# Performance work log

Hardware: AMD Instinct MI355X
Metric: run time of the kernel (lower is better)

## Reference

```python
import jax, jax.numpy as jnp
import numpy as np

B, L, G, K, HID, CLS = 256, 1000, 300, 19, 100, 2  # batch, seq len, num_cnns, kernel, per-unit hidden, classes
P = L // 10  # pooled length = per-group input features = 100
EPS = 1e-5


def setup_inputs() -> dict:
    key = jax.random.key(0)
    ks = jax.random.split(key, 24)
    u = lambda k, s: jax.random.uniform(k, s, jnp.float32, 0.5, 1.5)
    n = lambda k, s, sc=0.1: jax.random.normal(k, s, jnp.float32) * sc
    return {
        "x": jax.random.normal(ks[0], (B, 4, L), jnp.float32),
        # motif scanner conv: [out=G, in=4, k=19]
        "conv_w": n(ks[1], (G, 4, K)),
        "conv_b": n(ks[2], (G,)),
        "bn1_g": u(ks[3], (G,)), "bn1_b": n(ks[4], (G,)),
        "bn1_m": n(ks[5], (G,)), "bn1_v": u(ks[6], (G,)),
        # grouped 1x1 conv #1: per-group [HID <- P]
        "W1": n(ks[7], (G, HID, P)),
        "b1": n(ks[8], (G, HID)),
        "bn2_g": u(ks[9], (G, HID)), "bn2_b": n(ks[10], (G, HID)),
        "bn2_m": n(ks[11], (G, HID)), "bn2_v": u(ks[12], (G, HID)),
        # grouped 1x1 conv #2: per-group [1 <- HID]
        "W2": n(ks[13], (G, HID)),
        "b2": n(ks[14], (G,)),
        "bn3_g": u(ks[15], (G,)), "bn3_b": n(ks[16], (G,)),
        "bn3_m": n(ks[17], (G,)), "bn3_v": u(ks[18], (G,)),
        # final classifier Linear(G, CLS)
        "cls_w": n(ks[19], (CLS, G)),
        "cls_b": n(ks[20], (CLS,)),
    }


def reference(x, conv_w, conv_b, bn1_g, bn1_b, bn1_m, bn1_v,
              W1, b1, bn2_g, bn2_b, bn2_m, bn2_v,
              W2, b2, bn3_g, bn3_b, bn3_m, bn3_v,
              cls_w, cls_b):
    # Conv1d(4->G, k=19, pad=9): same-length output [B, G, L]
    h = jax.lax.conv_general_dilated(
        x, conv_w, window_strides=(1,), padding=[(K // 2, K // 2)],
        dimension_numbers=("NCH", "OIH", "NCH")) + conv_b[None, :, None]
    # BatchNorm1d (inference) + ReLU
    s1 = bn1_g / jnp.sqrt(bn1_v + EPS)
    h = jax.nn.relu((h - bn1_m[None, :, None]) * s1[None, :, None] + bn1_b[None, :, None])
    # MaxPool1d(10): L divisible by 10 -> reshape-max  [B, G, P]
    h = h.reshape(B, G, P, 10).max(-1)
    # Flatten+Unsqueeze+grouped 1x1 conv == block-diagonal matmul per group
    h1 = jnp.einsum("bgi,ghi->bgh", h, W1) + b1            # [B, G, HID]
    h1 = jax.nn.relu((h1 - bn2_m) * (bn2_g / jnp.sqrt(bn2_v + EPS)) + bn2_b)
    # Dropout(0.3) is identity at inference
    h2 = jnp.einsum("bgh,gh->bg", h1, W2) + b2             # [B, G]
    h2 = jax.nn.relu((h2 - bn3_m) * (bn3_g / jnp.sqrt(bn3_v + EPS)) + bn3_b)
    # classifier
    return h2 @ cls_w.T + cls_b                            # [B, CLS]
```

## Files before the change

kernel.cpp:

```cpp
#include <hip/hip_runtime.h>


typedef unsigned short ushort_t;
typedef short short8 __attribute__((ext_vector_type(8)));
typedef float floatx4 __attribute__((ext_vector_type(4)));

constexpr float EPSf = 1e-5f;

__device__ __forceinline__ ushort_t f2bf(float f) {
    unsigned u = __float_as_uint(f);
    unsigned r = (u + 0x7FFFu + ((u >> 16) & 1u)) >> 16;
    return (ushort_t)r;
}

constexpr int T1_BLKS = 8320;
constexpr int T2_BLKS = 114;
constexpr int T3_BLKS = 4200;
__global__ __launch_bounds__(256) void prep_all(
    const float* __restrict__ x, const float* __restrict__ conv_w, const float* __restrict__ W1,
    ushort_t* __restrict__ xph, ushort_t* __restrict__ Wc, ushort_t* __restrict__ W1b)
{
    const int blk = blockIdx.x, t = threadIdx.x;
    if (blk < T1_BLKS) {
        int u = blk * 256 + t;
        int iu = u % 520, r = u / 520;
        int c = r & 3, phi = (r >> 2) & 3, b = r >> 4;
        int src = iu * 2 + phi - 9;
        const float* xb = x + b * 4000 + c * 1000;
        float v0 = ((unsigned)src < 1000u) ? xb[src] : 0.f;
        float v1 = ((unsigned)(src + 1) < 1000u) ? xb[src + 1] : 0.f;
        ((unsigned*)xph)[u] = (unsigned)f2bf(v0) | ((unsigned)f2bf(v1) << 16);
    } else if (blk < T1_BLKS + T2_BLKS) {
        int idx = (blk - T1_BLKS) * 256 + t;
        int j = idx & 7, g = (idx >> 3) % 304, kc = idx / (304 * 8);
        int k = kc * 8 + j, c = k / 24, tt = k - c * 24;
        float v = (g < 300 && tt < 19) ? conv_w[g * 76 + c * 19 + tt] : 0.f;
        Wc[idx] = f2bf(v);
    } else {
        int v = (blk - T1_BLKS - T2_BLKS) * 256 + t;
        int jj = v & 1, r = v >> 1;
        int h = r % 112, r2 = r / 112;
        int kc = r2 & 15, g = r2 >> 4;
        int i0 = kc * 8 + jj * 4;
        ushort4 o = make_ushort4(0, 0, 0, 0);
        if (h < 100 && i0 <= 96) {
            float4 w = *(const float4*)&W1[(size_t)g * 10000 + h * 100 + i0];
            o = make_ushort4(f2bf(w.x), f2bf(w.y), f2bf(w.z), f2bf(w.w));
        }
        *(ushort4*)&W1b[((size_t)(g * 16 + kc) * 112 + h) * 8 + jj * 4] = o;
    }
}

__global__ __launch_bounds__(448, 2) void conv_mfma(
    const ushort_t* __restrict__ xph, const ushort_t* __restrict__ Wc,
    const float* __restrict__ conv_b, const float* __restrict__ g1, const float* __restrict__ be1,
    const float* __restrict__ m1, const float* __restrict__ v1,
    ushort_t* __restrict__ pooled)
{
    __shared__ ushort_t Wl[12 * 304 * 8];
    __shared__ ushort_t xl[16 * 1040];
    __shared__ float A1s[304], B1s[304];

    const int tid = threadIdx.x;
    const int b = blockIdx.x;

    {
        const uint4* wsrc = (const uint4*)Wc;
        uint4* wdst = (uint4*)Wl;
        for (int i = tid; i < 3648; i += 448) wdst[i] = wsrc[i];
        const uint4* xsrc = (const uint4*)(xph + (size_t)b * 16640);
        uint4* xdst = (uint4*)xl;
        for (int i = tid; i < 2080; i += 448) xdst[i] = xsrc[i];
        if (tid < 304) {
            if (tid < 300) {
                float A = g1[tid] * rsqrtf(v1[tid] + EPSf);
                A1s[tid] = A;
                B1s[tid] = (conv_b[tid] - m1[tid]) * A + be1[tid];
            } else { A1s[tid] = 0.f; B1s[tid] = 0.f; }
        }
    }
    __syncthreads();

    const int w = tid >> 6, lane = tid & 63;
    const int p0 = w * 16;
    const int row = lane & 15, quad = lane >> 4;
    const int p_r = p0 + row;
    const int prc = (p_r < 100) ? p_r : 99;

    uint4 af[10][3];
#pragma unroll
    for (int s = 0; s < 3; ++s) {
        int k0 = s * 32 + quad * 8;
        int c = k0 / 24, t0 = k0 - c * 24;
        int base0 = 10 * prc + t0;
        const ushort_t* xc = &xl[c * 1040];
#pragma unroll
        for (int d = 0; d < 10; ++d) {
            int base = base0 + d;
            int phi = base & 3, bi = base - phi;
            const ushort_t* p = xc + phi * 4160 + bi;
            uint2 lo = *(const uint2*)p;
            uint2 hi = *(const uint2*)(p + 4);
            af[d][s] = (uint4){lo.x, lo.y, hi.x, hi.y};
        }
    }

    for (int gt = 0; gt < 19; ++gt) {
        short8 bf[3];
#pragma unroll
        for (int s = 0; s < 3; ++s) {
            uint4 t4 = *(const uint4*)&Wl[(((s * 4 + quad) * 304) + gt * 16 + row) * 8];
            bf[s] = __builtin_bit_cast(short8, t4);
        }
        const float a1v = A1s[gt * 16 + row], b1v = B1s[gt * 16 + row];
        floatx4 mx = {0.f, 0.f, 0.f, 0.f};
#pragma unroll
        for (int d = 0; d < 10; ++d) {
            floatx4 acc = {0.f, 0.f, 0.f, 0.f};
#pragma unroll
            for (int s = 0; s < 3; ++s)
                acc = __builtin_amdgcn_mfma_f32_16x16x32_bf16(
                    __builtin_bit_cast(short8, af[d][s]), bf[s], acc, 0, 0, 0);
#pragma unroll
            for (int r = 0; r < 4; ++r)
                mx[r] = fmaxf(mx[r], fmaf(acc[r], a1v, b1v));
        }
        const int g = gt * 16 + row;
        const int pr0 = p0 + quad * 4;
        if (g < 300 && pr0 < 100) {
            ushort4 o = make_ushort4(f2bf(mx[0]), f2bf(mx[1]), f2bf(mx[2]), f2bf(mx[3]));
            *(ushort4*)&pooled[((size_t)b * 300 + g) * 100 + pr0] = o;
        }
    }
}

__global__ __launch_bounds__(256, 2) void mlp_mfma(
    const ushort_t* __restrict__ pooled, const ushort_t* __restrict__ W1b,
    const float* __restrict__ b1, const float* __restrict__ g2, const float* __restrict__ be2,
    const float* __restrict__ m2, const float* __restrict__ v2,
    const float* __restrict__ W2, const float* __restrict__ b2,
    const float* __restrict__ g3, const float* __restrict__ be3,
    const float* __restrict__ m3, const float* __restrict__ v3,
    float* __restrict__ h2ws)
{
    __shared__ ushort_t W1l[16 * 112 * 8];
    __shared__ ushort_t pl[128 * 128];
    __shared__ float A2s[112], C2s[112], w2sl[112];
    __shared__ float sA3, sC3;

    const int tid = threadIdx.x;
    const int g = blockIdx.y, b0 = blockIdx.x * 128;

    {
        const uint4* src = (const uint4*)(W1b + (size_t)g * 14336);
        uint4* dst = (uint4*)W1l;
        for (int i = tid; i < 1792; i += 256) dst[i] = src[i];
    }
    for (int q = tid; q < 128 * 16; q += 256) {
        int bl = q >> 4, kc = q & 15;
        const ushort_t* src = pooled + ((size_t)(b0 + bl) * 300 + g) * 100 + kc * 8;
        uint2 lo = *(const uint2*)src;
        uint2 hi = *(const uint2*)(src + 4);
        int swz = kc ^ (bl & 7);
        *(uint4*)&pl[((bl * 16) + swz) * 8] = (uint4){lo.x, lo.y, hi.x, hi.y};
    }
    if (tid < 112) {
        float a2 = 0.f, c2 = 0.f, w2v = 0.f;
        if (tid < 100) {
            int q = g * 100 + tid;
            a2 = g2[q] * rsqrtf(v2[q] + EPSf);
            c2 = (b1[q] - m2[q]) * a2 + be2[q];
            w2v = W2[q];
        }
        A2s[tid] = a2; C2s[tid] = c2; w2sl[tid] = w2v;
    }
    if (tid == 0) {
        float a3 = g3[g] * rsqrtf(v3[g] + EPSf);
        sA3 = a3; sC3 = (b2[g] - m3[g]) * a3 + be3[g];
    }
    __syncthreads();

    const int w = tid >> 6, lane = tid & 63;
    const int col = lane & 15, quad = lane >> 4;

    short8 bfr[7][4];
#pragma unroll
    for (int nt = 0; nt < 7; ++nt)
#pragma unroll
        for (int s = 0; s < 4; ++s) {
            uint4 t4 = *(const uint4*)&W1l[(((s * 4 + quad) * 112) + nt * 16 + col) * 8];
            bfr[nt][s] = __builtin_bit_cast(short8, t4);
        }

#pragma unroll
    for (int mi = 0; mi < 2; ++mi) {
        const int mt = w * 2 + mi;
        const int bl = mt * 16 + col;
        uint4 afr[4];
#pragma unroll
        for (int s = 0; s < 4; ++s) {
            int kc = s * 4 + quad;
            afr[s] = *(const uint4*)&pl[((bl * 16) + (kc ^ (bl & 7))) * 8];
        }
        float run0 = 0.f, run1 = 0.f, run2 = 0.f, run3 = 0.f;
#pragma unroll
        for (int nt = 0; nt < 7; ++nt) {
            floatx4 acc = {0.f, 0.f, 0.f, 0.f};
#pragma unroll
            for (int s = 0; s < 4; ++s)
                acc = __builtin_amdgcn_mfma_f32_16x16x32_bf16(
                    __builtin_bit_cast(short8, afr[s]), bfr[nt][s], acc, 0, 0, 0);
            const float a2v = A2s[nt * 16 + col], c2v = C2s[nt * 16 + col], w2v = w2sl[nt * 16 + col];
            run0 += fmaxf(fmaf(acc[0], a2v, c2v), 0.f) * w2v;
            run1 += fmaxf(fmaf(acc[1], a2v, c2v), 0.f) * w2v;
            run2 += fmaxf(fmaf(acc[2], a2v, c2v), 0.f) * w2v;
            run3 += fmaxf(fmaf(acc[3], a2v, c2v), 0.f) * w2v;
        }
#pragma unroll
        for (int m = 1; m <= 8; m <<= 1) {
            run0 += __shfl_xor(run0, m, 64);
            run1 += __shfl_xor(run1, m, 64);
            run2 += __shfl_xor(run2, m, 64);
            run3 += __shfl_xor(run3, m, 64);
        }
        if (col == 0) {
            float4 o;
            o.x = fmaxf(fmaf(run0, sA3, sC3), 0.f);
            o.y = fmaxf(fmaf(run1, sA3, sC3), 0.f);
            o.z = fmaxf(fmaf(run2, sA3, sC3), 0.f);
            o.w = fmaxf(fmaf(run3, sA3, sC3), 0.f);
            *(float4*)&h2ws[g * 256 + b0 + mt * 16 + quad * 4] = o;
        }
    }
}

__global__ __launch_bounds__(64) void classifier_kernel(
    const float* __restrict__ h2ws, const float* __restrict__ cls_w,
    const float* __restrict__ cls_b, float* __restrict__ out) {
    const int b = blockIdx.x, t = threadIdx.x;
    float a0 = 0.f, a1 = 0.f;
    for (int gg = t; gg < 300; gg += 64) {
        float v = h2ws[gg * 256 + b];
        a0 = fmaf(v, cls_w[gg], a0);
        a1 = fmaf(v, cls_w[300 + gg], a1);
    }
#pragma unroll
    for (int off = 32; off; off >>= 1) {
        a0 += __shfl_down(a0, off);
        a1 += __shfl_down(a1, off);
    }
    if (t == 0) {
        out[b * 2 + 0] = a0 + cls_b[0];
        out[b * 2 + 1] = a1 + cls_b[1];
    }
}

extern "C" void kernel_launch(void* const* d_in, const int* in_sizes, int n_in,
                              void* d_out, int out_size, void* d_ws, size_t ws_size,
                              hipStream_t stream) {
    const float* x      = (const float*)d_in[0];
    const float* conv_w = (const float*)d_in[1];
    const float* conv_b = (const float*)d_in[2];
    const float* bn1_g  = (const float*)d_in[3];
    const float* bn1_b  = (const float*)d_in[4];
    const float* bn1_m  = (const float*)d_in[5];
    const float* bn1_v  = (const float*)d_in[6];
    const float* W1     = (const float*)d_in[7];
    const float* b1     = (const float*)d_in[8];
    const float* bn2_g  = (const float*)d_in[9];
    const float* bn2_b  = (const float*)d_in[10];
    const float* bn2_m  = (const float*)d_in[11];
    const float* bn2_v  = (const float*)d_in[12];
    const float* W2     = (const float*)d_in[13];
    const float* b2     = (const float*)d_in[14];
    const float* bn3_g  = (const float*)d_in[15];
    const float* bn3_b  = (const float*)d_in[16];
    const float* bn3_m  = (const float*)d_in[17];
    const float* bn3_v  = (const float*)d_in[18];
    const float* cls_w  = (const float*)d_in[19];
    const float* cls_b  = (const float*)d_in[20];

    char* wsb = (char*)d_ws;
    ushort_t* pooled = (ushort_t*)(wsb);
    ushort_t* xph    = (ushort_t*)(wsb + 15360000);
    ushort_t* Wc     = (ushort_t*)(wsb + 23879680);
    ushort_t* W1b    = (ushort_t*)(wsb + 23938048);
    float*    h2ws   = (float*)  (wsb + 32539648);

    prep_all<<<dim3(T1_BLKS + T2_BLKS + T3_BLKS), 256, 0, stream>>>(x, conv_w, W1, xph, Wc, W1b);

    conv_mfma<<<dim3(256), 448, 0, stream>>>(
        xph, Wc, conv_b, bn1_g, bn1_b, bn1_m, bn1_v, pooled);

    mlp_mfma<<<dim3(2, 300), 256, 0, stream>>>(
        pooled, W1b, b1, bn2_g, bn2_b, bn2_m, bn2_v, W2, b2,
        bn3_g, bn3_b, bn3_m, bn3_v, h2ws);

    classifier_kernel<<<dim3(256), 64, 0, stream>>>(h2ws, cls_w, cls_b, (float*)d_out);
}
```

Before: 152.2 us.

## Fuse input phase-split into conv kernel, split conv over two halves, XCD-aware block mapping

The bf16 phase-split of x now happens inside the conv kernel, so the global xph intermediate and its large prep pass are gone. Each batch's conv work is split across two blocks along the pooled axis (52 and 48 positions), using 256 threads and a smaller LDS tile, which gives twice as many blocks. The W1 prep and MLP kernels remap block indices so that all blocks for one group land on the same XCD, aiming for L2 reuse of W1b and pooled data. The cost is some redundant x loads at the halo overlap and some idle blocks and wavefronts in the XCD mapping and the second conv half.

```diff
diff --git a/kernel.cpp b/kernel.cpp
--- a/kernel.cpp
+++ b/kernel.cpp
@@ -13,34 +13,28 @@
     return (ushort_t)r;
 }
 
-constexpr int T1_BLKS = 8320;
-constexpr int T2_BLKS = 114;
-constexpr int T3_BLKS = 4200;
+constexpr int WC_BLKS  = 114;
+constexpr int W1B_BLKS = 4256;
 __global__ __launch_bounds__(256) void prep_all(
-    const float* __restrict__ x, const float* __restrict__ conv_w, const float* __restrict__ W1,
-    ushort_t* __restrict__ xph, ushort_t* __restrict__ Wc, ushort_t* __restrict__ W1b)
+    const float* __restrict__ conv_w, const float* __restrict__ W1,
+    ushort_t* __restrict__ Wc, ushort_t* __restrict__ W1b)
 {
     const int blk = blockIdx.x, t = threadIdx.x;
-    if (blk < T1_BLKS) {
-        int u = blk * 256 + t;
-        int iu = u % 520, r = u / 520;
-        int c = r & 3, phi = (r >> 2) & 3, b = r >> 4;
-        int src = iu * 2 + phi - 9;
-        const float* xb = x + b * 4000 + c * 1000;
-        float v0 = ((unsigned)src < 1000u) ? xb[src] : 0.f;
-        float v1 = ((unsigned)(src + 1) < 1000u) ? xb[src + 1] : 0.f;
-        ((unsigned*)xph)[u] = (unsigned)f2bf(v0) | ((unsigned)f2bf(v1) << 16);
-    } else if (blk < T1_BLKS + T2_BLKS) {
-        int idx = (blk - T1_BLKS) * 256 + t;
+    if (blk < WC_BLKS) {
+        int idx = blk * 256 + t;
         int j = idx & 7, g = (idx >> 3) % 304, kc = idx / (304 * 8);
         int k = kc * 8 + j, c = k / 24, tt = k - c * 24;
         float v = (g < 300 && tt < 19) ? conv_w[g * 76 + c * 19 + tt] : 0.f;
         Wc[idx] = f2bf(v);
     } else {
-        int v = (blk - T1_BLKS - T2_BLKS) * 256 + t;
+        int blk2 = blk - WC_BLKS;
+        int xcd = blk2 & 7, j = blk2 >> 3;
+        int gl = j / 14, inner = j - gl * 14;
+        int g = xcd * 38 + gl;
+        if (g >= 300) return;
+        int v = inner * 256 + t;
         int jj = v & 1, r = v >> 1;
-        int h = r % 112, r2 = r / 112;
-        int kc = r2 & 15, g = r2 >> 4;
+        int h = r % 112, kc = r / 112;
         int i0 = kc * 8 + jj * 4;
         ushort4 o = make_ushort4(0, 0, 0, 0);
         if (h < 100 && i0 <= 96) {
@@ -51,54 +45,62 @@
     }
 }
 
-__global__ __launch_bounds__(448, 2) void conv_mfma(
-    const ushort_t* __restrict__ xph, const ushort_t* __restrict__ Wc,
+__global__ __launch_bounds__(256, 2) void conv_mfma(
+    const float* __restrict__ x, const ushort_t* __restrict__ Wc,
     const float* __restrict__ conv_b, const float* __restrict__ g1, const float* __restrict__ be1,
     const float* __restrict__ m1, const float* __restrict__ v1,
     ushort_t* __restrict__ pooled)
 {
     __shared__ ushort_t Wl[12 * 304 * 8];
-    __shared__ ushort_t xl[16 * 1040];
+    __shared__ ushort_t xl[16 * 552];
     __shared__ float A1s[304], B1s[304];
 
     const int tid = threadIdx.x;
-    const int b = blockIdx.x;
-
+    const int b = blockIdx.x, q = blockIdx.y;
+    const int X0 = q * 520;
+
+    for (int u = tid; u < 16 * 276; u += 256) {
+        int iu = u % 276, r = u / 276;
+        int c = r & 3, phi = r >> 2;
+        int gi = X0 + 2 * iu + phi - 9;
+        const float* xb = x + b * 4000 + c * 1000;
+        float v0 = ((unsigned)gi < 1000u) ? xb[gi] : 0.f;
+        float v1_ = ((unsigned)(gi + 1) < 1000u) ? xb[gi + 1] : 0.f;
+        ((unsigned*)xl)[u] = (unsigned)f2bf(v0) | ((unsigned)f2bf(v1_) << 16);
+    }
     {
         const uint4* wsrc = (const uint4*)Wc;
         uint4* wdst = (uint4*)Wl;
-        for (int i = tid; i < 3648; i += 448) wdst[i] = wsrc[i];
-        const uint4* xsrc = (const uint4*)(xph + (size_t)b * 16640);
-        uint4* xdst = (uint4*)xl;
-        for (int i = tid; i < 2080; i += 448) xdst[i] = xsrc[i];
-        if (tid < 304) {
-            if (tid < 300) {
-                float A = g1[tid] * rsqrtf(v1[tid] + EPSf);
-                A1s[tid] = A;
-                B1s[tid] = (conv_b[tid] - m1[tid]) * A + be1[tid];
-            } else { A1s[tid] = 0.f; B1s[tid] = 0.f; }
-        }
+        for (int i = tid; i < 3648; i += 256) wdst[i] = wsrc[i];
+    }
+    for (int i = tid; i < 304; i += 256) {
+        if (i < 300) {
+            float A = g1[i] * rsqrtf(v1[i] + EPSf);
+            A1s[i] = A;
+            B1s[i] = (conv_b[i] - m1[i]) * A + be1[i];
+        } else { A1s[i] = 0.f; B1s[i] = 0.f; }
     }
     __syncthreads();
 
     const int w = tid >> 6, lane = tid & 63;
-    const int p0 = w * 16;
+    if (q == 1 && w == 3) return;
+    const int p0 = q ? (52 + w * 16) : (w * 16);
+    const int pmax = q ? 99 : 51;
     const int row = lane & 15, quad = lane >> 4;
     const int p_r = p0 + row;
-    const int prc = (p_r < 100) ? p_r : 99;
+    const int prc = (p_r < pmax) ? p_r : pmax;
 
     uint4 af[10][3];
 #pragma unroll
     for (int s = 0; s < 3; ++s) {
         int k0 = s * 32 + quad * 8;
         int c = k0 / 24, t0 = k0 - c * 24;
-        int base0 = 10 * prc + t0;
-        const ushort_t* xc = &xl[c * 1040];
+        int base0 = 10 * prc + t0 - X0;
 #pragma unroll
         for (int d = 0; d < 10; ++d) {
-            int base = base0 + d;
-            int phi = base & 3, bi = base - phi;
-            const ushort_t* p = xc + phi * 4160 + bi;
+            int local = base0 + d;
+            int phi = local & 3, bi = local - phi;
+            const ushort_t* p = &xl[(phi * 4 + c) * 552 + bi];
             uint2 lo = *(const uint2*)p;
             uint2 hi = *(const uint2*)(p + 4);
             af[d][s] = (uint4){lo.x, lo.y, hi.x, hi.y};
@@ -127,7 +129,7 @@
         }
         const int g = gt * 16 + row;
         const int pr0 = p0 + quad * 4;
-        if (g < 300 && pr0 < 100) {
+        if (g < 300 && pr0 + 3 <= pmax) {
             ushort4 o = make_ushort4(f2bf(mx[0]), f2bf(mx[1]), f2bf(mx[2]), f2bf(mx[3]));
             *(ushort4*)&pooled[((size_t)b * 300 + g) * 100 + pr0] = o;
         }
@@ -149,7 +151,11 @@
     __shared__ float sA3, sC3;
 
     const int tid = threadIdx.x;
-    const int g = blockIdx.y, b0 = blockIdx.x * 128;
+    const int blk = blockIdx.x;
+    const int xcd = blk & 7, j = blk >> 3;
+    const int g = xcd * 38 + (j >> 1);
+    if (g >= 300) return;
+    const int b0 = (j & 1) * 128;
 
     {
         const uint4* src = (const uint4*)(W1b + (size_t)g * 14336);
@@ -167,10 +173,10 @@
     if (tid < 112) {
         float a2 = 0.f, c2 = 0.f, w2v = 0.f;
         if (tid < 100) {
-            int q = g * 100 + tid;
-            a2 = g2[q] * rsqrtf(v2[q] + EPSf);
-            c2 = (b1[q] - m2[q]) * a2 + be2[q];
-            w2v = W2[q];
+            int qq = g * 100 + tid;
+            a2 = g2[qq] * rsqrtf(v2[qq] + EPSf);
+            c2 = (b1[qq] - m2[qq]) * a2 + be2[qq];
+            w2v = W2[qq];
         }
         A2s[tid] = a2; C2s[tid] = c2; w2sl[tid] = w2v;
     }
@@ -282,17 +288,16 @@
 
     char* wsb = (char*)d_ws;
     ushort_t* pooled = (ushort_t*)(wsb);
-    ushort_t* xph    = (ushort_t*)(wsb + 15360000);
-    ushort_t* Wc     = (ushort_t*)(wsb + 23879680);
-    ushort_t* W1b    = (ushort_t*)(wsb + 23938048);
-    float*    h2ws   = (float*)  (wsb + 32539648);
-
-    prep_all<<<dim3(T1_BLKS + T2_BLKS + T3_BLKS), 256, 0, stream>>>(x, conv_w, W1, xph, Wc, W1b);
-
-    conv_mfma<<<dim3(256), 448, 0, stream>>>(
-        xph, Wc, conv_b, bn1_g, bn1_b, bn1_m, bn1_v, pooled);
-
-    mlp_mfma<<<dim3(2, 300), 256, 0, stream>>>(
+    ushort_t* Wc     = (ushort_t*)(wsb + 15360000);
+    ushort_t* W1b    = (ushort_t*)(wsb + 15418368);
+    float*    h2ws   = (float*)  (wsb + 24019968);
+
+    prep_all<<<dim3(WC_BLKS + W1B_BLKS), 256, 0, stream>>>(conv_w, W1, Wc, W1b);
+
+    conv_mfma<<<dim3(256, 2), 256, 0, stream>>>(
+        x, Wc, conv_b, bn1_g, bn1_b, bn1_m, bn1_v, pooled);
+
+    mlp_mfma<<<dim3(608), 256, 0, stream>>>(
         pooled, W1b, b1, bn2_g, bn2_b, bn2_m, bn2_v, W2, b2,
         bn3_g, bn3_b, bn3_m, bn3_v, h2ws);
 
```

New measurement: 145.9 us. 4.2% less time.
